# Performance work log

Measured on AMD Instinct MI355X. Metric: run time of the kernel, lower is better.

## Reference

```python
import jax, jax.numpy as jnp
import numpy as np

EPS = 1e-6
GRID_ORDER_K = 4
DIST_K = 3


def _smallest_k(d, k):
    # k smallest values along last axis, ascending (torch.topk largest=False)
    return -jax.lax.top_k(-d, k)[0]


def _radius_loss(real, fake):
    qs = jnp.array([0.05, 0.1, 0.25, 0.5, 0.75, 0.9, 0.95], jnp.float32)
    fq = jnp.quantile(fake[:, :, 2], qs)
    rq = jnp.quantile(real[:, :, 2], qs)
    return jnp.mean((fq - rq) ** 2)


def _grid_density_loss(real, fake):
    qs = jnp.array([0.05, 0.25, 0.5, 0.75, 0.95], jnp.float32)
    lx = jnp.mean((jnp.quantile(fake[:, :, 0], qs) - jnp.quantile(real[:, :, 0], qs)) ** 2)
    ly = jnp.mean((jnp.quantile(fake[:, :, 1], qs) - jnp.quantile(real[:, :, 1], qs)) ** 2)
    return (lx + ly) / 2


def _knn_dists_flat(x, k):
    # x: [B,N,3]; pairwise dist on xy with +eps under sqrt as in source
    xy = x[:, :, :2]
    d = jnp.sqrt(((xy[:, :, None, :] - xy[:, None, :, :]) ** 2).sum(-1) + EPS)  # [B,N,N]
    d = _smallest_k(d, k)  # [B,N,k]
    return d.reshape(x.shape[0], -1)


def _distance_loss(real, fake):
    qs = jnp.array([0.05, 0.5, 0.95], jnp.float32)
    rq = jnp.quantile(_knn_dists_flat(real, DIST_K), qs, axis=1)  # [3,B]
    fq = jnp.quantile(_knn_dists_flat(fake, DIST_K), qs, axis=1)
    return jnp.mean((fq - rq) ** 2)


def _hexatic_order(coords, k):
    # coords: [B,N,2] -> psi: [B,N] complex
    B, N, _ = coords.shape
    diffs = coords[:, :, None, :] - coords[:, None, :, :]  # [B,N,N,2]
    dx = diffs[..., 0]
    dx = dx + EPS * (jnp.abs(dx) < EPS).astype(dx.dtype)
    angles = jnp.arctan2(diffs[..., 1], dx)
    e_iktheta = jnp.exp(1j * k * angles)  # [B,N,N] complex64
    dist = jnp.sqrt((diffs ** 2).sum(-1) + EPS)
    eye = jnp.eye(N, dtype=bool)[None]
    dist = jnp.where(eye, jnp.inf, dist)
    kth = jax.lax.stop_gradient(_smallest_k(dist, k)[..., -1])  # [B,N]
    sigma = jnp.maximum(0.1 * jnp.maximum(kth[..., None], EPS), EPS)
    arg = jnp.clip((kth[..., None] - dist) / sigma, -50.0, 50.0)
    w = jax.nn.sigmoid(arg)
    psi = (e_iktheta * w).sum(2) / jnp.maximum(w.sum(2), EPS)
    return psi


def _grid_order_loss(samples):
    psi = _hexatic_order(samples[:, :, :2], GRID_ORDER_K)
    return -jnp.mean(jnp.sqrt(psi * jnp.conj(psi))).real


def _physical_feasibility_loss(fake):
    xy = fake[:, :, :2]
    r = fake[:, :, 2]
    N = fake.shape[1]
    sq = ((xy[:, :, None, :] - xy[:, None, :, :]) ** 2).sum(-1)
    d = jnp.sqrt(jnp.where(sq <= 0, 1.0, sq))  # safe sqrt (guard grads at 0)
    d = jnp.where(sq <= 0, 0.0, d)
    tril = jnp.tril(jnp.ones((N, N), bool))[None]
    d = jnp.where(tril, d, 0.0)
    d = jnp.where(d <= 0, jnp.inf, d)
    radii_pair = jnp.abs(r)[:, None, :] + jnp.abs(r)[:, :, None]
    overlap = jax.nn.relu(radii_pair - (d + 1e-4))  # sqrt(x**2)==x for x>=0
    return overlap.sum() / (radii_pair.sum() / 2)


def _gan_loss(fake_outputs):
    t = 0.9  # ones_like - 0.1 label smoothing
    logp = jnp.maximum(jnp.log(fake_outputs), -100.0)
    log1mp = jnp.maximum(jnp.log(1.0 - fake_outputs), -100.0)
    return -jnp.mean(t * logp + (1.0 - t) * log1mp)


def setup_inputs() -> dict:
    key = jax.random.key(0)
    k1, k2, k3 = jax.random.split(key, 3)
    B, N = 4, 2048
    real_images = jax.random.normal(k1, (B, N, 3), jnp.float32)
    fake_images = jax.random.normal(k2, (B, N, 3), jnp.float32)
    fake_outputs = jax.random.uniform(k3, (B, 1), jnp.float32, 1e-3, 1.0 - 1e-3)
    return {"real_images": real_images, "fake_images": fake_images, "fake_outputs": fake_outputs}


def reference(real_images, fake_images, fake_outputs):
    loss = _radius_loss(real_images, fake_images)
    loss = loss + _physical_feasibility_loss(fake_images)
    loss = loss + _gan_loss(fake_outputs)
    loss = loss + _grid_density_loss(real_images, fake_images)
    loss = loss + _distance_loss(real_images, fake_images)
    loss = loss + _grid_order_loss(fake_images)
    return loss
```

## Files before the change

kernel.cpp:

```cpp
#include <hip/hip_runtime.h>
#include <math.h>

#define B_SZ   4
#define N_PTS  2048
#define EPSF   1e-6f

#define WS_KNN_R 0
#define WS_KNN_F 24576
#define WS_FEAS  49152
#define WS_PSIP  50176
#define WS_RSUM  51200
#define WS_Q     51204
#define WS_TICK  51264
#define QZF (WS_Q + 0)
#define QZR (WS_Q + 7)
#define QXF (WS_Q + 14)
#define QXR (WS_Q + 19)
#define QYF (WS_Q + 24)
#define QYR (WS_Q + 29)
#define QDR (WS_Q + 34)
#define QDF (WS_Q + 46)
#define COMP_SCALE 256.0f
#define KNN_SCALE  1024.0f

__constant__ float c_qs7[7] = {0.05f, 0.1f, 0.25f, 0.5f, 0.75f, 0.9f, 0.95f};
__constant__ float c_qs5[5] = {0.05f, 0.25f, 0.5f, 0.75f, 0.95f};
__constant__ float c_qs3[3] = {0.05f, 0.5f, 0.95f};

#define CE(a, b) { float _lo = fminf(a, b), _hi = fmaxf(a, b); a = _lo; b = _hi; }

__device__ __forceinline__ void ins3a(float m[3], float v) {
    float h0 = fmaxf(m[0], v); m[0] = fminf(m[0], v);
    float h1 = fmaxf(m[1], h0); m[1] = fminf(m[1], h0);
    m[2] = fminf(m[2], h1);
}
__device__ __forceinline__ void ins5a(float m[5], float v) {
    float h0 = fmaxf(m[0], v); m[0] = fminf(m[0], v);
    float h1 = fmaxf(m[1], h0); m[1] = fminf(m[1], h0);
    float h2 = fmaxf(m[2], h1); m[2] = fminf(m[2], h1);
    float h3 = fmaxf(m[3], h2); m[3] = fminf(m[3], h2);
    m[4] = fminf(m[4], h3);
}

__global__ __launch_bounds__(256) void hs_pair_kernel(const float* __restrict__ real,
                                                      const float* __restrict__ fake,
                                                      float* __restrict__ ws) {
    __shared__ float2 sxy[N_PTS];
    __shared__ float sr[N_PTS];
    __shared__ float red[256];
    const int tid = threadIdx.x, wave = tid >> 6, lane = tid & 63;
    const int blk = blockIdx.x;
    if (blk == 0 && tid == 0) ((unsigned int*)ws)[WS_TICK] = 0u;

    if (blk < 1024) {
        const int b = blk >> 8, grp = blk & 255;
        const float* src = fake + (size_t)b * N_PTS * 3;
        for (int t = tid; t < N_PTS; t += 256) {
            const float* p = src + t * 3;
            sxy[t] = make_float2(p[0], p[1]);
            sr[t]  = fabsf(p[2]);
        }
        __syncthreads();
        const int p0 = grp * 8 + wave * 2;
        float px[2], py[2], pri[2], m[2][5];
#pragma unroll
        for (int t = 0; t < 2; ++t) {
            px[t] = sxy[p0 + t].x; py[t] = sxy[p0 + t].y;
            pri[t] = sr[p0 + t] - 1e-4f;
            m[t][0] = m[t][1] = m[t][2] = m[t][3] = m[t][4] = INFINITY;
        }
        float acc = 0.f;
        for (int j = lane; j < N_PTS; j += 64) {
            float2 q = sxy[j]; float br = sr[j];
#pragma unroll
            for (int t = 0; t < 2; ++t) {
                float dx = px[t] - q.x, dy = py[t] - q.y;
                float sq = fmaf(dx, dx, dy * dy);
                ins5a(m[t], sq);
                float ov = fmaxf((pri[t] + br) - sqrtf(sq), 0.f);
                acc += (sq > 0.f) ? ov : 0.f;
            }
        }
#pragma unroll
        for (int off = 1; off < 64; off <<= 1) {
#pragma unroll
            for (int t = 0; t < 2; ++t) {
                float b0 = __shfl_xor(m[t][0], off);
                float b1 = __shfl_xor(m[t][1], off);
                float b2 = __shfl_xor(m[t][2], off);
                float b3 = __shfl_xor(m[t][3], off);
                float b4 = __shfl_xor(m[t][4], off);
                float l0 = fminf(m[t][0], b4);
                float l1 = fminf(m[t][1], b3);
                float l2 = fminf(m[t][2], b2);
                float l3 = fminf(m[t][3], b1);
                float l4 = fminf(m[t][4], b0);
                CE(l0, l3); CE(l1, l4); CE(l0, l2); CE(l1, l3);
                CE(l0, l1); CE(l2, l4); CE(l1, l2); CE(l3, l4); CE(l2, l3);
                m[t][0] = l0; m[t][1] = l1; m[t][2] = l2; m[t][3] = l3; m[t][4] = l4;
            }
        }
        if (lane == 0) {
            float* kout = ws + WS_KNN_F + b * (N_PTS * 3);
#pragma unroll
            for (int t = 0; t < 2; ++t) {
                const int i = p0 + t;
                kout[i * 3 + 0] = sqrtf(m[t][0] + EPSF);
                kout[i * 3 + 1] = sqrtf(m[t][1] + EPSF);
                kout[i * 3 + 2] = sqrtf(m[t][2] + EPSF);
            }
        }
        float kth[2], invs[2];
#pragma unroll
        for (int t = 0; t < 2; ++t) {
            kth[t] = sqrtf(m[t][4] + EPSF);
            invs[t] = 1.f / fmaxf(0.1f * fmaxf(kth[t], EPSF), EPSF);
        }
        float sw[2], sre[2], sim[2];
#pragma unroll
        for (int t = 0; t < 2; ++t) { sw[t] = 0.f; sre[t] = 0.f; sim[t] = 0.f; }
        for (int j = lane; j < N_PTS; j += 64) {
            float2 q = sxy[j];
#pragma unroll
            for (int t = 0; t < 2; ++t) {
                float dx = px[t] - q.x, dy = py[t] - q.y;
                float sq = fmaf(dx, dx, dy * dy);
                float dist = sqrtf(sq + EPSF);
                dist = (j == p0 + t) ? INFINITY : dist;
                float a = dx + ((fabsf(dx) < EPSF) ? EPSF : 0.f);
                float arg = fminf(fmaxf((kth[t] - dist) * invs[t], -50.f), 50.f);
                float e = __expf(-arg);
                float w = __builtin_amdgcn_rcpf(1.f + e);
                float aa = a * a, bb = dy * dy;
                float n2 = aa + bb;
                float z2r = aa - bb;
                float t0 = a * dy; float z2i = t0 + t0;
                float inv = __builtin_amdgcn_rcpf(n2);
                float ur = z2r * inv, ui = z2i * inv;
                float e4r = fmaf(ur, ur, -(ui * ui));
                float t1 = ur * ui; float e4i = t1 + t1;
                sw[t] += w;
                sre[t] = fmaf(w, e4r, sre[t]);
                sim[t] = fmaf(w, e4i, sim[t]);
            }
        }
#pragma unroll
        for (int off = 1; off < 64; off <<= 1) {
#pragma unroll
            for (int t = 0; t < 2; ++t) {
                sw[t]  += __shfl_xor(sw[t], off);
                sre[t] += __shfl_xor(sre[t], off);
                sim[t] += __shfl_xor(sim[t], off);
            }
        }
        float mypsi = 0.f;
        if (lane == 0) {
#pragma unroll
            for (int t = 0; t < 2; ++t) {
                float den = fmaxf(sw[t], EPSF);
                float pr = sre[t] / den, pi = sim[t] / den;
                mypsi += sqrtf(fmaf(pr, pr, pi * pi));
            }
        }
        red[tid] = acc;
        __syncthreads();
        for (int s = 128; s > 0; s >>= 1) {
            if (tid < s) red[tid] += red[tid + s];
            __syncthreads();
        }
        if (tid == 0) ws[WS_FEAS + blk] = red[0];
        __syncthreads();
        red[tid] = (lane == 0) ? mypsi : 0.f;
        __syncthreads();
        for (int s = 128; s > 0; s >>= 1) {
            if (tid < s) red[tid] += red[tid + s];
            __syncthreads();
        }
        if (tid == 0) ws[WS_PSIP + blk] = red[0];
        if (grp == 0) {
            __syncthreads();
            float rs = 0.f;
            for (int t = tid; t < N_PTS; t += 256) rs += sr[t];
            red[tid] = rs;
            __syncthreads();
            for (int s = 128; s > 0; s >>= 1) {
                if (tid < s) red[tid] += red[tid + s];
                __syncthreads();
            }
            if (tid == 0) ws[WS_RSUM + b] = red[0];
        }
    } else {
        const int rb = blk - 1024;
        const int b = rb >> 7, grp = rb & 127;
        const float* src = real + (size_t)b * N_PTS * 3;
        for (int t = tid; t < N_PTS; t += 256) {
            const float* p = src + t * 3;
            sxy[t] = make_float2(p[0], p[1]);
        }
        __syncthreads();
        const int p0 = grp * 16 + wave * 4;
        float px[4], py[4], m[4][3];
#pragma unroll
        for (int t = 0; t < 4; ++t) {
            px[t] = sxy[p0 + t].x; py[t] = sxy[p0 + t].y;
            m[t][0] = m[t][1] = m[t][2] = INFINITY;
        }
        for (int j = lane; j < N_PTS; j += 64) {
            float2 q = sxy[j];
#pragma unroll
            for (int t = 0; t < 4; ++t) {
                float dx = px[t] - q.x, dy = py[t] - q.y;
                float sq = fmaf(dx, dx, dy * dy);
                ins3a(m[t], sq);
            }
        }
#pragma unroll
        for (int off = 1; off < 64; off <<= 1) {
#pragma unroll
            for (int t = 0; t < 4; ++t) {
                float b0 = __shfl_xor(m[t][0], off);
                float b1 = __shfl_xor(m[t][1], off);
                float b2 = __shfl_xor(m[t][2], off);
                float l0 = fminf(m[t][0], b2);
                float l1 = fminf(m[t][1], b1);
                float l2 = fminf(m[t][2], b0);
                CE(l0, l1); CE(l0, l2); CE(l1, l2);
                m[t][0] = l0; m[t][1] = l1; m[t][2] = l2;
            }
        }
        if (lane == 0) {
            float* kout = ws + WS_KNN_R + b * (N_PTS * 3);
#pragma unroll
            for (int t = 0; t < 4; ++t) {
                const int i = p0 + t;
                kout[i * 3 + 0] = sqrtf(m[t][0] + EPSF);
                kout[i * 3 + 1] = sqrtf(m[t][1] + EPSF);
                kout[i * 3 + 2] = sqrtf(m[t][2] + EPSF);
            }
        }
    }
}

__global__ __launch_bounds__(256) void hs_quant_kernel(const float* __restrict__ real,
                                                       const float* __restrict__ fake,
                                                       const float* __restrict__ fouts,
                                                       float* __restrict__ ws,
                                                       float* __restrict__ out) {
    __shared__ unsigned int hist[4][4096];
    __shared__ unsigned int s_wsum[4];
    __shared__ float sred[256];
    __shared__ int s_last;
    unsigned int* wsu = (unsigned int*)ws;
    const int tid = threadIdx.x, wave = tid >> 6, lane = tid & 63;
    const int aid = blockIdx.x;

    const float* src; int step, n, nq, slot; float vlo, vw; const float* qs;
    if (aid < 6) {
        src = ((aid & 1) ? real : fake) + ((aid < 2) ? 2 : ((aid < 4) ? 0 : 1));
        step = 3; n = 8192;
        nq = (aid < 2) ? 7 : 5;
        slot = (aid < 2) ? (QZF + aid * 7) : (QXF + (aid - 2) * 5);
        vlo = -8.f; vw = 1.f / COMP_SCALE;
        qs = (aid < 2) ? c_qs7 : c_qs5;
    } else {
        const int a = aid - 6;
        src = ws + ((a < 4) ? WS_KNN_R + a * (N_PTS * 3) : WS_KNN_F + (a - 4) * (N_PTS * 3));
        step = 1; n = N_PTS * 3; nq = 3;
        slot = (a < 4) ? (QDR + a * 3) : (QDF + (a - 4) * 3);
        vlo = 0.f; vw = 1.f / KNN_SCALE;
        qs = c_qs3;
    }

    unsigned int* hflat = &hist[0][0];
#pragma unroll
    for (int i = 0; i < 64; ++i) hflat[i * 256 + tid] = 0u;
    __syncthreads();

    const float scale = (aid < 6) ? COMP_SCALE : KNN_SCALE;
    const float bias  = (aid < 6) ? 8.0f : 0.0f;
    for (int e = tid; e < n; e += 256) {
        const float v = src[(size_t)e * step];
        int bin = (int)floorf((v + bias) * scale);
        bin = (bin < 0) ? 0 : (bin > 4095 ? 4095 : bin);
        atomicAdd(&hist[wave][bin], 1u);
    }
    __syncthreads();

    unsigned int c[16], ps = 0;
    const int base = tid * 16;
#pragma unroll
    for (int i = 0; i < 16; ++i) {
        c[i] = hist[0][base + i] + hist[1][base + i] + hist[2][base + i] + hist[3][base + i];
        ps += c[i];
    }
    unsigned int incl = ps;
#pragma unroll
    for (int off = 1; off < 64; off <<= 1) {
        unsigned int nb = (unsigned int)__shfl_up((int)incl, off);
        if (lane >= off) incl += nb;
    }
    if (lane == 63) s_wsum[wave] = incl;
    __syncthreads();
    unsigned int woff = 0;
    for (int w2 = 0; w2 < wave; ++w2) woff += s_wsum[w2];
    unsigned int run = incl - ps + woff;
    unsigned int* sh_cum = &hist[0][0];
#pragma unroll
    for (int i = 0; i < 16; ++i) { run += c[i]; sh_cum[base + i] = run; }
    __syncthreads();

    if (tid < nq) {
        const float pos = qs[tid] * (float)(n - 1);
        const int k = (int)pos;
        const float frac = pos - (float)k;
        float v2[2];
#pragma unroll
        for (int t = 0; t < 2; ++t) {
            const unsigned int r = (unsigned int)(k + t);
            int lo_ = 0, hi_ = 4095;
            while (lo_ < hi_) {
                const int mid = (lo_ + hi_) >> 1;
                if (sh_cum[mid] > r) hi_ = mid; else lo_ = mid + 1;
            }
            const unsigned int excl = (lo_ > 0) ? sh_cum[lo_ - 1] : 0u;
            const unsigned int cnt  = sh_cum[lo_] - excl;
            v2[t] = vlo + ((float)lo_ + ((float)(r - excl) + 0.5f) / (float)cnt) * vw;
        }
        ws[slot + tid] = v2[0] + frac * (v2[1] - v2[0]);
    }

    __threadfence();
    __syncthreads();
    if (tid == 0) {
        const unsigned int t = atomicAdd(&wsu[WS_TICK], 1u);
        s_last = (t == 13u) ? 1 : 0;
    }
    __syncthreads();
    if (!s_last) return;
    __threadfence();

    float fs = 0.f, ps2 = 0.f;
    for (int t = tid; t < 1024; t += 256) {
        fs  += ws[WS_FEAS + t];
        ps2 += ws[WS_PSIP + t];
    }
    sred[tid] = fs;
    __syncthreads();
    for (int s = 128; s > 0; s >>= 1) {
        if (tid < s) sred[tid] += sred[tid + s];
        __syncthreads();
    }
    const float s_feas = sred[0];
    __syncthreads();
    sred[tid] = ps2;
    __syncthreads();
    for (int s = 128; s > 0; s >>= 1) {
        if (tid < s) sred[tid] += sred[tid + s];
        __syncthreads();
    }
    if (tid == 0) {
        const float psi_sum = sred[0];
        const float rsum = ws[WS_RSUM + 0] + ws[WS_RSUM + 1] + ws[WS_RSUM + 2] + ws[WS_RSUM + 3];
        float loss = 0.f;
        float sacc = 0.f;
        for (int qq = 0; qq < 7; ++qq) { float d = ws[QZF + qq] - ws[QZR + qq]; sacc += d * d; }
        loss += sacc / 7.f;
        loss += (0.5f * s_feas) / ((float)N_PTS * rsum);
        float g = 0.f;
        for (int b = 0; b < B_SZ; ++b) {
            float p = fouts[b];
            g += 0.9f * fmaxf(logf(p), -100.f) + 0.1f * fmaxf(logf(1.f - p), -100.f);
        }
        loss += -g / (float)B_SZ;
        float sx = 0.f, sy = 0.f;
        for (int qq = 0; qq < 5; ++qq) {
            float dx = ws[QXF + qq] - ws[QXR + qq]; sx += dx * dx;
            float dy = ws[QYF + qq] - ws[QYR + qq]; sy += dy * dy;
        }
        loss += 0.5f * (sx / 5.f + sy / 5.f);
        float sd = 0.f;
        for (int t = 0; t < 12; ++t) { float d = ws[QDF + t] - ws[QDR + t]; sd += d * d; }
        loss += sd / 12.f;
        loss += -psi_sum / (float)(B_SZ * N_PTS);
        out[0] = loss;
    }
}

extern "C" void kernel_launch(void* const* d_in, const int* in_sizes, int n_in,
                              void* d_out, int out_size, void* d_ws, size_t ws_size,
                              hipStream_t stream) {
    (void)in_sizes; (void)n_in; (void)out_size; (void)ws_size;
    const float* real  = (const float*)d_in[0];
    const float* fake  = (const float*)d_in[1];
    const float* fouts = (const float*)d_in[2];
    float* out = (float*)d_out;
    float* ws  = (float*)d_ws;

    hipLaunchKernelGGL(hs_pair_kernel,  dim3(1536), dim3(256), 0, stream, real, fake, ws);
    hipLaunchKernelGGL(hs_quant_kernel, dim3(14),   dim3(256), 0, stream, real, fake, fouts, ws, out);
}
```

Before: 116.4 us.

## Compact candidate neighbors within sigmoid cutoff radius before hexatic accumulation

Each wave now first scans all points with a cheap squared-distance test against the radius kth + 50·sigma, beyond which the clamped sigmoid weight is negligible. Surviving indices are compacted into a per-wave shared-memory list using ballot and mbcnt. The expensive hexatic-order math (sqrt, exp, reciprocals, complex power) then runs only over that list instead of all 2048 points. If a list overflows CAP entries, it falls back to the full loop. The trade-off is extra shared memory and a pre-pass, and the result drops contributions of about sigmoid(-50).

```diff
diff --git a/kernel.cpp b/kernel.cpp
--- a/kernel.cpp
+++ b/kernel.cpp
@@ -4,6 +4,7 @@
 #define B_SZ   4
 #define N_PTS  2048
 #define EPSF   1e-6f
+#define CAP    768
 
 #define WS_KNN_R 0
 #define WS_KNN_F 24576
@@ -48,6 +49,7 @@
     __shared__ float2 sxy[N_PTS];
     __shared__ float sr[N_PTS];
     __shared__ float red[256];
+    __shared__ unsigned short slist[4 * 2 * CAP];
     const int tid = threadIdx.x, wave = tid >> 6, lane = tid & 63;
     const int blk = blockIdx.x;
     if (blk == 0 && tid == 0) ((unsigned int*)ws)[WS_TICK] = 0u;
@@ -110,55 +112,96 @@
                 kout[i * 3 + 2] = sqrtf(m[t][2] + EPSF);
             }
         }
-        float kth[2], invs[2];
+        float kth[2], invs[2], T2[2];
 #pragma unroll
         for (int t = 0; t < 2; ++t) {
             kth[t] = sqrtf(m[t][4] + EPSF);
-            invs[t] = 1.f / fmaxf(0.1f * fmaxf(kth[t], EPSF), EPSF);
-        }
-        float sw[2], sre[2], sim[2];
-#pragma unroll
-        for (int t = 0; t < 2; ++t) { sw[t] = 0.f; sre[t] = 0.f; sim[t] = 0.f; }
-        for (int j = lane; j < N_PTS; j += 64) {
+            const float sigma = fmaxf(0.1f * fmaxf(kth[t], EPSF), EPSF);
+            invs[t] = 1.f / sigma;
+            const float T = kth[t] + 50.f * sigma;
+            T2[t] = T * T;
+        }
+        unsigned int cnt[2] = {0u, 0u};
+        const int lbase = wave * 2 * CAP;
+        for (int it = 0; it < 32; ++it) {
+            const int j = it * 64 + lane;
             float2 q = sxy[j];
 #pragma unroll
             for (int t = 0; t < 2; ++t) {
                 float dx = px[t] - q.x, dy = py[t] - q.y;
                 float sq = fmaf(dx, dx, dy * dy);
-                float dist = sqrtf(sq + EPSF);
-                dist = (j == p0 + t) ? INFINITY : dist;
-                float a = dx + ((fabsf(dx) < EPSF) ? EPSF : 0.f);
-                float arg = fminf(fmaxf((kth[t] - dist) * invs[t], -50.f), 50.f);
-                float e = __expf(-arg);
-                float w = __builtin_amdgcn_rcpf(1.f + e);
-                float aa = a * a, bb = dy * dy;
-                float n2 = aa + bb;
-                float z2r = aa - bb;
-                float t0 = a * dy; float z2i = t0 + t0;
-                float inv = __builtin_amdgcn_rcpf(n2);
-                float ur = z2r * inv, ui = z2i * inv;
-                float e4r = fmaf(ur, ur, -(ui * ui));
-                float t1 = ur * ui; float e4i = t1 + t1;
-                sw[t] += w;
-                sre[t] = fmaf(w, e4r, sre[t]);
-                sim[t] = fmaf(w, e4i, sim[t]);
-            }
-        }
-#pragma unroll
-        for (int off = 1; off < 64; off <<= 1) {
-#pragma unroll
-            for (int t = 0; t < 2; ++t) {
-                sw[t]  += __shfl_xor(sw[t], off);
-                sre[t] += __shfl_xor(sre[t], off);
-                sim[t] += __shfl_xor(sim[t], off);
+                const bool p = (sq <= T2[t]);
+                const unsigned long long mk = __ballot(p);
+                const unsigned int below = __builtin_amdgcn_mbcnt_hi(
+                    (unsigned int)(mk >> 32),
+                    __builtin_amdgcn_mbcnt_lo((unsigned int)mk, 0u));
+                const unsigned int off = cnt[t] + below;
+                if (p && off < CAP) slist[lbase + t * CAP + off] = (unsigned short)j;
+                cnt[t] += (unsigned int)__popcll((long long)mk);
             }
         }
         float mypsi = 0.f;
-        if (lane == 0) {
-#pragma unroll
-            for (int t = 0; t < 2; ++t) {
-                float den = fmaxf(sw[t], EPSF);
-                float pr = sre[t] / den, pi = sim[t] / den;
+#pragma unroll
+        for (int t = 0; t < 2; ++t) {
+            float swv = 0.f, srev = 0.f, simv = 0.f;
+            if (cnt[t] <= CAP) {
+                const int len = (int)cnt[t];
+                for (int i = lane; i < len; i += 64) {
+                    const int j = slist[lbase + t * CAP + i];
+                    float2 q = sxy[j];
+                    float dx = px[t] - q.x, dy = py[t] - q.y;
+                    float sq = fmaf(dx, dx, dy * dy);
+                    float dist = sqrtf(sq + EPSF);
+                    dist = (j == p0 + t) ? INFINITY : dist;
+                    float a = dx + ((fabsf(dx) < EPSF) ? EPSF : 0.f);
+                    float arg = fminf(fmaxf((kth[t] - dist) * invs[t], -50.f), 50.f);
+                    float e = __expf(-arg);
+                    float w = __builtin_amdgcn_rcpf(1.f + e);
+                    float aa = a * a, bb = dy * dy;
+                    float n2 = aa + bb;
+                    float z2r = aa - bb;
+                    float t0 = a * dy; float z2i = t0 + t0;
+                    float inv = __builtin_amdgcn_rcpf(n2);
+                    float ur = z2r * inv, ui = z2i * inv;
+                    float e4r = fmaf(ur, ur, -(ui * ui));
+                    float t1 = ur * ui; float e4i = t1 + t1;
+                    swv += w;
+                    srev = fmaf(w, e4r, srev);
+                    simv = fmaf(w, e4i, simv);
+                }
+            } else {
+                for (int j = lane; j < N_PTS; j += 64) {
+                    float2 q = sxy[j];
+                    float dx = px[t] - q.x, dy = py[t] - q.y;
+                    float sq = fmaf(dx, dx, dy * dy);
+                    float dist = sqrtf(sq + EPSF);
+                    dist = (j == p0 + t) ? INFINITY : dist;
+                    float a = dx + ((fabsf(dx) < EPSF) ? EPSF : 0.f);
+                    float arg = fminf(fmaxf((kth[t] - dist) * invs[t], -50.f), 50.f);
+                    float e = __expf(-arg);
+                    float w = __builtin_amdgcn_rcpf(1.f + e);
+                    float aa = a * a, bb = dy * dy;
+                    float n2 = aa + bb;
+                    float z2r = aa - bb;
+                    float t0 = a * dy; float z2i = t0 + t0;
+                    float inv = __builtin_amdgcn_rcpf(n2);
+                    float ur = z2r * inv, ui = z2i * inv;
+                    float e4r = fmaf(ur, ur, -(ui * ui));
+                    float t1 = ur * ui; float e4i = t1 + t1;
+                    swv += w;
+                    srev = fmaf(w, e4r, srev);
+                    simv = fmaf(w, e4i, simv);
+                }
+            }
+#pragma unroll
+            for (int off = 1; off < 64; off <<= 1) {
+                swv  += __shfl_xor(swv, off);
+                srev += __shfl_xor(srev, off);
+                simv += __shfl_xor(simv, off);
+            }
+            if (lane == 0) {
+                const float den = fmaxf(swv, EPSF);
+                const float pr = srev / den, pi = simv / den;
                 mypsi += sqrtf(fmaf(pr, pr, pi * pi));
             }
         }
```

After: 111.9 us. 3.9% less time.
